# Kernel tuning notes

Hardware: AMD Instinct MI355X
Metric: run time of the kernel (lower is better)

Reference implementation:

```python
import jax, jax.numpy as jnp
import numpy as np

HEAD_SIZE = 128
N_EMBED = 2048
B, T = 4, 4096


def setup_inputs() -> dict:
    key = jax.random.key(0)
    kx, kq, kk, kv = jax.random.split(key, 4)
    s = 1.0 / np.sqrt(N_EMBED)
    return {
        "x": jax.random.normal(kx, (B, T, N_EMBED), dtype=jnp.float32),
        "Wq": jax.random.normal(kq, (N_EMBED, HEAD_SIZE), dtype=jnp.float32) * s,
        "Wk": jax.random.normal(kk, (N_EMBED, HEAD_SIZE), dtype=jnp.float32) * s,
        "Wv": jax.random.normal(kv, (N_EMBED, HEAD_SIZE), dtype=jnp.float32) * s,
    }


def reference(x, Wq, Wk, Wv):
    # x: [B, T, C]; projections (no bias)
    q = jnp.einsum('btc,cd->btd', x, Wq)  # [B, T, D]
    k = jnp.einsum('btc,cd->btd', x, Wk)
    v = jnp.einsum('btc,cd->btd', x, Wv)
    scale = q.shape[-1] ** -0.5
    scores = jnp.einsum('btd,bsd->bts', q, k) * scale  # [B, T, T]
    T_ = x.shape[1]
    causal = jnp.tril(jnp.ones((T_, T_), dtype=bool))
    scores = jnp.where(causal, scores, -jnp.inf)
    weight = jax.nn.softmax(scores, axis=-1)
    # dropout is identity in eval mode
    out = jnp.einsum('bts,bsd->btd', weight, v)  # [B, T, D]
    return out
```

## Files before the change

### kernel.cpp

```cpp
#include <hip/hip_runtime.h>
#include <hip/hip_bf16.h>
#include <stdint.h>

typedef unsigned short ushort_t;
typedef short v8s __attribute__((ext_vector_type(8)));
typedef float f32x4 __attribute__((ext_vector_type(4)));
typedef float f32x16 __attribute__((ext_vector_type(16)));

#define MFMA16(a, b, c) __builtin_amdgcn_mfma_f32_16x16x32_bf16(a, b, c, 0, 0, 0)
#define MFMA32(a, b, c) __builtin_amdgcn_mfma_f32_32x32x16_bf16(a, b, c, 0, 0, 0)

typedef __attribute__((address_space(1))) void gvoid;
typedef __attribute__((address_space(3))) void svoid;

__device__ __forceinline__ void gld16(const void* g, void* s) {
    __builtin_amdgcn_global_load_lds((gvoid*)g, (svoid*)s, 16, 0, 0);
}

__device__ __forceinline__ ushort_t f2bf(float f) {
    union { __hip_bfloat16 b; ushort_t u; } c;
    c.b = __float2bfloat16(f);
    return c.u;
}

__device__ __forceinline__ unsigned f2bf2(float a, float b) {
    union { __hip_bfloat162 b2; unsigned u; } c;
    c.b2 = __float22bfloat162_rn(make_float2(a, b));
    return c.u;
}

__global__ void transpose_w(const float* __restrict__ Wq, const float* __restrict__ Wk,
                            const float* __restrict__ Wv, ushort_t* __restrict__ WT) {
    __shared__ float tile[64][132];
    int bid = blockIdx.x;
    int w = bid >> 5;
    int k0 = (bid & 31) << 6;
    const float* W = (w == 0) ? Wq : ((w == 1) ? Wk : Wv);
    int tid = threadIdx.x;
    #pragma unroll
    for (int i = 0; i < 8; i++) {
        int row = i * 8 + (tid >> 5);
        int col = (tid & 31) * 4;
        float4 v = *(const float4*)(W + (size_t)(k0 + row) * 128 + col);
        tile[row][col] = v.x; tile[row][col + 1] = v.y;
        tile[row][col + 2] = v.z; tile[row][col + 3] = v.w;
    }
    __syncthreads();
    int n = tid >> 1, kh = (tid & 1) * 32;
    ushort_t* dst = WT + ((size_t)(w * 128 + n)) * 2048 + k0 + kh;
    #pragma unroll
    for (int j = 0; j < 32; j += 4) {
        union { ushort_t u[4]; uint2 v2; } pk;
        #pragma unroll
        for (int e = 0; e < 4; e++) pk.u[e] = f2bf(tile[kh + j + e][n]);
        *(uint2*)(dst + j) = pk.v2;
    }
}

#define PJ_XLOAD(S, IT)                                                       \
    {                                                                         \
        _Pragma("unroll")                                                     \
        for (int i = 0; i < 4; i++)                                           \
            S[i] = *(const f32x4*)(xsrc[i] + (size_t)(IT) * 256);             \
    }

#define PJ_CVT_WRITE(RS, PAR)                                                 \
    {                                                                         \
        _Pragma("unroll")                                                     \
        for (int i = 0; i < 4; i++) {                                         \
            uint2 p;                                                          \
            p.x = f2bf2(RS[i][0], RS[i][1]);                                  \
            p.y = f2bf2(RS[i][2], RS[i][3]);                                  \
            *(uint2*)((char*)abuf + (PAR) * 16384 + awb[i]) = p;              \
        }                                                                     \
    }

#define PJ_PHASE1(PAR, IT, DOB)                                               \
    {                                                                         \
        const char* ab = (const char*)abuf + (PAR) * 16384;                   \
        const char* bb = (const char*)bbuf + (PAR) * 24576;                   \
        v8s af[4], bf[3];                                                     \
        _Pragma("unroll")                                                     \
        for (int m = 0; m < 4; m++) {                                         \
            int row = wr * 64 + m * 16 + lr;                                  \
            af[m] = *(const v8s*)(ab + row * 128 + ((lg * 16) ^ ((row & 7) << 4))); \
        }                                                                     \
        _Pragma("unroll")                                                     \
        for (int n = 0; n < 3; n++) {                                         \
            int row = wc * 48 + n * 16 + lr;                                  \
            bf[n] = *(const v8s*)(bb + row * 128 + ((lg * 16) ^ ((row & 7) << 4))); \
        }                                                                     \
        __builtin_amdgcn_sched_barrier(0);                                    \
        if (DOB) {                                                            \
            _Pragma("unroll")                                                 \
            for (int i = 0; i < 3; i++)                                       \
                gld16(bsrc[i] + (size_t)((IT) + 1) * 128,                     \
                      (char*)bbuf + ((PAR) ^ 1) * 24576 + (wid * 3 + i) * 1024); \
        }                                                                     \
        __builtin_amdgcn_sched_barrier(0);                                    \
        __builtin_amdgcn_s_barrier();                                         \
        asm volatile("s_waitcnt lgkmcnt(0)" ::: "memory");                    \
        __builtin_amdgcn_sched_barrier(0);                                    \
        __builtin_amdgcn_s_setprio(1);                                        \
        _Pragma("unroll")                                                     \
        for (int m = 0; m < 4; m++)                                           \
            _Pragma("unroll")                                                 \
            for (int n = 0; n < 3; n++)                                       \
                acc[m][n] = MFMA16(af[m], bf[n], acc[m][n]);                  \
        __builtin_amdgcn_s_setprio(0);                                        \
        __builtin_amdgcn_s_barrier();                                         \
    }

#define PJ_PHASE2(PAR, IT, RLOAD, RCVT, DOX, DOB)                             \
    {                                                                         \
        const char* ab = (const char*)abuf + (PAR) * 16384;                   \
        const char* bb = (const char*)bbuf + (PAR) * 24576;                   \
        v8s af[4], bf[3];                                                     \
        _Pragma("unroll")                                                     \
        for (int m = 0; m < 4; m++) {                                         \
            int row = wr * 64 + m * 16 + lr;                                  \
            af[m] = *(const v8s*)(ab + row * 128 + ((64 + lg * 16) ^ ((row & 7) << 4))); \
        }                                                                     \
        _Pragma("unroll")                                                     \
        for (int n = 0; n < 3; n++) {                                         \
            int row = wc * 48 + n * 16 + lr;                                  \
            bf[n] = *(const v8s*)(bb + row * 128 + ((64 + lg * 16) ^ ((row & 7) << 4))); \
        }                                                                     \
        __builtin_amdgcn_sched_barrier(0);                                    \
        if (DOX) PJ_XLOAD(RLOAD, (IT) + 2);                                   \
        __builtin_amdgcn_sched_barrier(0);                                    \
        if (DOB) PJ_CVT_WRITE(RCVT, (PAR) ^ 1);                               \
        __builtin_amdgcn_sched_barrier(0);                                    \
        if (DOB) {                                                            \
            if (DOX) { asm volatile("s_waitcnt vmcnt(4)" ::: "memory"); }     \
            else     { asm volatile("s_waitcnt vmcnt(0)" ::: "memory"); }     \
        }                                                                     \
        __builtin_amdgcn_s_barrier();                                         \
        asm volatile("s_waitcnt lgkmcnt(0)" ::: "memory");                    \
        __builtin_amdgcn_sched_barrier(0);                                    \
        __builtin_amdgcn_s_setprio(1);                                        \
        _Pragma("unroll")                                                     \
        for (int m = 0; m < 4; m++)                                           \
            _Pragma("unroll")                                                 \
            for (int n = 0; n < 3; n++)                                       \
                acc[m][n] = MFMA16(af[m], bf[n], acc[m][n]);                  \
        __builtin_amdgcn_s_setprio(0);                                        \
        __builtin_amdgcn_s_barrier();                                         \
    }

#define PJ_TILE(PAR, IT, RLOAD, RCVT, DOX, DOB)                               \
    PJ_PHASE1(PAR, IT, DOB)                                                   \
    PJ_PHASE2(PAR, IT, RLOAD, RCVT, DOX, DOB)

__launch_bounds__(512, 1)
__global__ void proj_kernel(const float* __restrict__ x, const ushort_t* __restrict__ WT,
                            ushort_t* __restrict__ q, ushort_t* __restrict__ kb,
                            ushort_t* __restrict__ vb) {
    __shared__ ushort_t abuf[2][8192];
    __shared__ ushort_t bbuf[2][12288];

    int bid = blockIdx.x;
    int xcd = bid & 7, t2 = bid >> 3;
    int nh = t2 & 1, mtl = t2 >> 1;
    int mtile = xcd * 16 + mtl;
    size_t m0 = (size_t)mtile * 128;
    int c0 = nh * 192;
    int tid = threadIdx.x, lane = tid & 63, wid = tid >> 6;
    int lg = lane >> 4, lr = lane & 15;
    int wr = wid >> 2, wc = wid & 3;

    f32x4 acc[4][3];
    #pragma unroll
    for (int m = 0; m < 4; m++)
        #pragma unroll
        for (int n = 0; n < 3; n++) acc[m][n] = (f32x4){0.f, 0.f, 0.f, 0.f};

    const char* xsrc[4];
    int awb[4];
    #pragma unroll
    for (int i = 0; i < 4; i++) {
        int row = 16 * wid + 4 * i + (lane >> 4);
        xsrc[i] = (const char*)x + (m0 + row) * 8192 + (lane & 15) * 16;
        awb[i] = row * 128 + (((lane & 15) * 8) ^ ((row & 7) << 4));
    }

    const char* bsrc[3];
    #pragma unroll
    for (int i = 0; i < 3; i++) {
        int row = 8 * (3 * wid + i) + (lane >> 3);
        int col = ((lane & 7) * 16) ^ ((row & 7) << 4);
        bsrc[i] = (const char*)WT + (size_t)(c0 + row) * 4096 + col;
    }

    f32x4 xs0[4], xs1[4];
    #pragma unroll
    for (int i = 0; i < 3; i++)
        gld16(bsrc[i], (char*)bbuf + (wid * 3 + i) * 1024);
    PJ_XLOAD(xs0, 0);
    PJ_XLOAD(xs1, 1);
    PJ_CVT_WRITE(xs0, 0);
    asm volatile("s_waitcnt vmcnt(0)" ::: "memory");
    asm volatile("s_waitcnt lgkmcnt(0)" ::: "memory");
    __builtin_amdgcn_s_barrier();

    for (int t = 0; t < 30; t += 2) {
        PJ_TILE(0, t,     xs0, xs1, 1, 1);
        PJ_TILE(1, t + 1, xs1, xs0, 1, 1);
    }
    PJ_TILE(0, 30, xs0, xs1, 0, 1);
    PJ_TILE(1, 31, xs1, xs0, 0, 0);

    #pragma unroll
    for (int m = 0; m < 4; m++) {
        #pragma unroll
        for (int e = 0; e < 4; e++) {
            size_t row = m0 + (size_t)(wr * 64 + m * 16 + 4 * lg + e);
            int t = (int)(row & 4095);
            size_t base = (row >> 12) * 524288;
            #pragma unroll
            for (int n = 0; n < 3; n++) {
                int col = c0 + wc * 48 + n * 16 + lr;
                int w = col >> 7, d = col & 127;
                ushort_t val = f2bf(acc[m][n][e]);
                if (w == 0)
                    q[base + (size_t)(t >> 5) * 4096 + (d >> 4) * 512 + ((d >> 3) & 1) * 256 + (t & 31) * 8 + (d & 7)] = val;
                else if (w == 1)
                    kb[base + (size_t)(t >> 5) * 4096 + (d >> 4) * 512 + ((d >> 3) & 1) * 256 + (t & 31) * 8 + (d & 7)] = val;
                else
                    vb[base + (size_t)(t >> 4) * 2048 + (d >> 5) * 512 + ((t >> 3) & 1) * 256 + (d & 31) * 8 + (t & 7)] = val;
            }
        }
    }
}

__device__ __forceinline__ f32x16 zero16() {
    f32x16 z;
    #pragma unroll
    for (int i = 0; i < 16; i++) z[i] = 0.f;
    return z;
}

#define ATT_PVC(SV, BASE, VC, CNEXT)                                          \
    {                                                                         \
        unsigned a0 = f2bf2(SV[(BASE) + 0], SV[(BASE) + 1]);                  \
        unsigned a1 = f2bf2(SV[(BASE) + 2], SV[(BASE) + 3]);                  \
        unsigned b0 = f2bf2(SV[(BASE) + 4], SV[(BASE) + 5]);                  \
        unsigned b1 = f2bf2(SV[(BASE) + 6], SV[(BASE) + 7]);                  \
        unsigned snd0 = hi ? a0 : b0, snd1 = hi ? a1 : b1;                    \
        unsigned rcv0 = (unsigned)__shfl_xor((int)snd0, 32);                  \
        unsigned rcv1 = (unsigned)__shfl_xor((int)snd1, 32);                  \
        union { unsigned u[4]; v8s v; } pf;                                   \
        pf.u[0] = hi ? rcv0 : a0;                                             \
        pf.u[1] = hi ? rcv1 : a1;                                             \
        pf.u[2] = hi ? b0 : rcv0;                                             \
        pf.u[3] = hi ? b1 : rcv1;                                             \
        __builtin_amdgcn_s_setprio(1);                                        \
        _Pragma("unroll")                                                     \
        for (int dt = 0; dt < 4; dt++)                                        \
            accO[dt] = MFMA32(VC[dt], pf.v, accO[dt]);                        \
        __builtin_amdgcn_s_setprio(0);                                        \
        if ((CNEXT) >= 0) {                                                   \
            _Pragma("unroll")                                                 \
            for (int dt = 0; dt < 4; dt++)                                    \
                VC[dt] = *(const v8s*)(vg + (CNEXT) * 2048 + dt * 512);       \
        }                                                                     \
    }

__launch_bounds__(256, 2)
__global__ void attn_kernel(const ushort_t* __restrict__ q, const ushort_t* __restrict__ kb,
                            const ushort_t* __restrict__ vb, float* __restrict__ out) {
    __shared__ float obuf[4][4][16][64];
    __shared__ float stat[2][4][64];

    int bid = blockIdx.x;
    int xcd = bid & 7, rk = bid >> 3;
    int b = xcd >> 1;
    int g = rk * 2 + (xcd & 1);
    int qt = (g & 1) ? (g >> 1) : (127 - (g >> 1));
    int qt0 = qt * 32;
    int tid = threadIdx.x, lane = tid & 63, wid = tid >> 6;
    int hi = lane >> 5, lo = lane & 31;
    size_t bb = (size_t)b * 524288;
    int nt = (qt >> 1) + 1;
    const float cexp = 0.08838834764831845f * 1.4426950408889634f;

    v8s qf[8];
    {
        const ushort_t* qg = q + bb + (size_t)qt * 4096 + (size_t)lane * 8;
        #pragma unroll
        for (int ks = 0; ks < 8; ks++) qf[ks] = *(const v8s*)(qg + ks * 512);
    }

    f32x16 accO[4];
    #pragma unroll
    for (int dt = 0; dt < 4; dt++) accO[dt] = zero16();
    float mrun = -1e30f, lrun = 0.f;

    for (int t = wid; t < nt; t += 4) {
        const ushort_t* kg = kb + bb + (size_t)t * 8192 + (size_t)lane * 8;
        const ushort_t* vg = vb + bb + (size_t)t * 8192 + (size_t)lane * 8;

        f32x16 s0 = zero16(), s1 = zero16();
        __builtin_amdgcn_s_setprio(1);
        #pragma unroll
        for (int ks = 0; ks < 8; ks++) {
            v8s kf = *(const v8s*)(kg + ks * 512);
            s0 = MFMA32(kf, qf[ks], s0);
        }
        #pragma unroll
        for (int ks = 0; ks < 8; ks++) {
            v8s kf = *(const v8s*)(kg + 4096 + ks * 512);
            s1 = MFMA32(kf, qf[ks], s1);
        }
        __builtin_amdgcn_s_setprio(0);

        v8s vA[4], vB[4];
        #pragma unroll
        for (int dt = 0; dt < 4; dt++) vA[dt] = *(const v8s*)(vg + dt * 512);
        #pragma unroll
        for (int dt = 0; dt < 4; dt++) vB[dt] = *(const v8s*)(vg + 2048 + dt * 512);

        if (t == nt - 1) {
            int qrow = qt0 + lo;
            #pragma unroll
            for (int r = 0; r < 16; r++) {
                int kvb = t * 64 + (r & 3) + 8 * (r >> 2) + 4 * hi;
                if (kvb > qrow) s0[r] = -1e30f;
                if (kvb + 32 > qrow) s1[r] = -1e30f;
            }
        }

        float mx = s0[0];
        #pragma unroll
        for (int r = 1; r < 16; r++) mx = fmaxf(mx, s0[r]);
        #pragma unroll
        for (int r = 0; r < 16; r++) mx = fmaxf(mx, s1[r]);
        mx = fmaxf(mx, __shfl_xor(mx, 32));

        if (__any(mx > mrun + 62.7f)) {
            float mnew = fmaxf(mrun, mx);
            float fr = exp2f((mrun - mnew) * cexp);
            lrun *= fr;
            #pragma unroll
            for (int dt = 0; dt < 4; dt++)
                #pragma unroll
                for (int r = 0; r < 16; r++) accO[dt][r] *= fr;
            mrun = mnew;
        }
        float mc = mrun * cexp;
        float rs = 0.f;
        #pragma unroll
        for (int r = 0; r < 16; r++) { s0[r] = exp2f(fmaf(s0[r], cexp, -mc)); rs += s0[r]; }
        #pragma unroll
        for (int r = 0; r < 16; r++) { s1[r] = exp2f(fmaf(s1[r], cexp, -mc)); rs += s1[r]; }
        rs += __shfl_xor(rs, 32);
        lrun += rs;

        ATT_PVC(s0, 0, vA, 2);
        ATT_PVC(s0, 8, vB, 3);
        ATT_PVC(s1, 0, vA, -1);
        ATT_PVC(s1, 8, vB, -1);
    }

    #pragma unroll
    for (int dt = 0; dt < 4; dt++)
        #pragma unroll
        for (int r = 0; r < 16; r++)
            obuf[wid][dt][r][lane] = accO[dt][r];
    stat[0][wid][lane] = mrun;
    stat[1][wid][lane] = lrun;
    __syncthreads();

    float m0 = stat[0][0][lane], m1 = stat[0][1][lane];
    float m2 = stat[0][2][lane], m3 = stat[0][3][lane];
    float m = fmaxf(fmaxf(m0, m1), fmaxf(m2, m3));
    float f0 = exp2f((m0 - m) * cexp), f1 = exp2f((m1 - m) * cexp);
    float f2 = exp2f((m2 - m) * cexp), f3 = exp2f((m3 - m) * cexp);
    float lsum = f0 * stat[1][0][lane] + f1 * stat[1][1][lane]
               + f2 * stat[1][2][lane] + f3 * stat[1][3][lane];
    float linv = 1.0f / lsum;

    float o[16];
    #pragma unroll
    for (int r = 0; r < 16; r++)
        o[r] = (f0 * obuf[0][wid][r][lane] + f1 * obuf[1][wid][r][lane]
              + f2 * obuf[2][wid][r][lane] + f3 * obuf[3][wid][r][lane]) * linv;

    float* orow = out + ((size_t)b * 4096 + qt0 + lo) * 128 + wid * 32 + 4 * hi;
    #pragma unroll
    for (int a = 0; a < 4; a++) {
        float4 vv;
        vv.x = o[4 * a + 0]; vv.y = o[4 * a + 1];
        vv.z = o[4 * a + 2]; vv.w = o[4 * a + 3];
        *(float4*)(orow + 8 * a) = vv;
    }
}

extern "C" void kernel_launch(void* const* d_in, const int* in_sizes, int n_in,
                              void* d_out, int out_size, void* d_ws, size_t ws_size,
                              hipStream_t stream) {
    const float* x  = (const float*)d_in[0];
    const float* Wq = (const float*)d_in[1];
    const float* Wk = (const float*)d_in[2];
    const float* Wv = (const float*)d_in[3];
    float* out = (float*)d_out;
    char* ws = (char*)d_ws;

    ushort_t* q  = (ushort_t*)(ws);
    ushort_t* kb = (ushort_t*)(ws + (4u << 20));
    ushort_t* vb = (ushort_t*)(ws + (8u << 20));
    ushort_t* WT = (ushort_t*)(ws + (12u << 20));

    transpose_w<<<dim3(96), dim3(256), 0, stream>>>(Wq, Wk, Wv, WT);
    proj_kernel<<<dim3(256), dim3(512), 0, stream>>>(x, WT, q, kb, vb);
    attn_kernel<<<dim3(512), dim3(256), 0, stream>>>(q, kb, vb, out);
}
```

Before: 91.83 us.

## Triple-buffer weight tiles in projection GEMM to prefetch two iterations ahead

The projection kernel's weight (B) tiles move from a double buffer to a triple buffer in LDS, and each iteration now issues their async global-to-LDS loads two k-steps ahead instead of one. The vmcnt wait is relaxed to allow more outstanding loads, and the bf16 convert-write of x is reordered to follow the wait. The aim is to hide global load latency for the weights behind more MFMA work. The cost is an extra 24 KB of LDS and a more intricate slot rotation that has to stay consistent with the wait counts.

```diff
diff --git a/kernel.cpp b/kernel.cpp
--- a/kernel.cpp
+++ b/kernel.cpp
@@ -75,10 +75,10 @@
         }                                                                     \
     }
 
-#define PJ_PHASE1(PAR, IT, DOB)                                               \
+#define PJ_PHASE1(APAR, BSLOT, BNSLOT, IT, DOB2)                              \
     {                                                                         \
-        const char* ab = (const char*)abuf + (PAR) * 16384;                   \
-        const char* bb = (const char*)bbuf + (PAR) * 24576;                   \
+        const char* ab = (const char*)abuf + (APAR) * 16384;                  \
+        const char* bb = (const char*)bbuf + (BSLOT) * 24576;                 \
         v8s af[4], bf[3];                                                     \
         _Pragma("unroll")                                                     \
         for (int m = 0; m < 4; m++) {                                         \
@@ -91,11 +91,11 @@
             bf[n] = *(const v8s*)(bb + row * 128 + ((lg * 16) ^ ((row & 7) << 4))); \
         }                                                                     \
         __builtin_amdgcn_sched_barrier(0);                                    \
-        if (DOB) {                                                            \
+        if (DOB2) {                                                           \
             _Pragma("unroll")                                                 \
             for (int i = 0; i < 3; i++)                                       \
-                gld16(bsrc[i] + (size_t)((IT) + 1) * 128,                     \
-                      (char*)bbuf + ((PAR) ^ 1) * 24576 + (wid * 3 + i) * 1024); \
+                gld16(bsrc[i] + (size_t)((IT) + 2) * 128,                     \
+                      (char*)bbuf + (BNSLOT) * 24576 + (wid * 3 + i) * 1024); \
         }                                                                     \
         __builtin_amdgcn_sched_barrier(0);                                    \
         __builtin_amdgcn_s_barrier();                                         \
@@ -111,10 +111,10 @@
         __builtin_amdgcn_s_barrier();                                         \
     }
 
-#define PJ_PHASE2(PAR, IT, RLOAD, RCVT, DOX, DOB)                             \
+#define PJ_PHASE2(APAR, BSLOT, IT, RLOAD, RCVT, DOX2, DOCVT, VMN)             \
     {                                                                         \
-        const char* ab = (const char*)abuf + (PAR) * 16384;                   \
-        const char* bb = (const char*)bbuf + (PAR) * 24576;                   \
+        const char* ab = (const char*)abuf + (APAR) * 16384;                  \
+        const char* bb = (const char*)bbuf + (BSLOT) * 24576;                 \
         v8s af[4], bf[3];                                                     \
         _Pragma("unroll")                                                     \
         for (int m = 0; m < 4; m++) {                                         \
@@ -127,14 +127,13 @@
             bf[n] = *(const v8s*)(bb + row * 128 + ((64 + lg * 16) ^ ((row & 7) << 4))); \
         }                                                                     \
         __builtin_amdgcn_sched_barrier(0);                                    \
-        if (DOX) PJ_XLOAD(RLOAD, (IT) + 2);                                   \
-        __builtin_amdgcn_sched_barrier(0);                                    \
-        if (DOB) PJ_CVT_WRITE(RCVT, (PAR) ^ 1);                               \
-        __builtin_amdgcn_sched_barrier(0);                                    \
-        if (DOB) {                                                            \
-            if (DOX) { asm volatile("s_waitcnt vmcnt(4)" ::: "memory"); }     \
-            else     { asm volatile("s_waitcnt vmcnt(0)" ::: "memory"); }     \
-        }                                                                     \
+        if (DOX2) PJ_XLOAD(RLOAD, (IT) + 2);                                  \
+        __builtin_amdgcn_sched_barrier(0);                                    \
+        if ((VMN) == 7) { asm volatile("s_waitcnt vmcnt(7)" ::: "memory"); }  \
+        else if ((VMN) == 0) { asm volatile("s_waitcnt vmcnt(0)" ::: "memory"); } \
+        __builtin_amdgcn_sched_barrier(0);                                    \
+        if (DOCVT) PJ_CVT_WRITE(RCVT, (APAR) ^ 1);                            \
+        __builtin_amdgcn_sched_barrier(0);                                    \
         __builtin_amdgcn_s_barrier();                                         \
         asm volatile("s_waitcnt lgkmcnt(0)" ::: "memory");                    \
         __builtin_amdgcn_sched_barrier(0);                                    \
@@ -148,16 +147,16 @@
         __builtin_amdgcn_s_barrier();                                         \
     }
 
-#define PJ_TILE(PAR, IT, RLOAD, RCVT, DOX, DOB)                               \
-    PJ_PHASE1(PAR, IT, DOB)                                                   \
-    PJ_PHASE2(PAR, IT, RLOAD, RCVT, DOX, DOB)
+#define PJ_TILE(APAR, BSLOT, BNSLOT, IT, RLOAD, RCVT, DOB2, DOX2, DOCVT, VMN) \
+    PJ_PHASE1(APAR, BSLOT, BNSLOT, IT, DOB2)                                  \
+    PJ_PHASE2(APAR, BSLOT, IT, RLOAD, RCVT, DOX2, DOCVT, VMN)
 
 __launch_bounds__(512, 1)
 __global__ void proj_kernel(const float* __restrict__ x, const ushort_t* __restrict__ WT,
                             ushort_t* __restrict__ q, ushort_t* __restrict__ kb,
                             ushort_t* __restrict__ vb) {
     __shared__ ushort_t abuf[2][8192];
-    __shared__ ushort_t bbuf[2][12288];
+    __shared__ ushort_t bbuf[3][12288];
 
     int bid = blockIdx.x;
     int xcd = bid & 7, t2 = bid >> 3;
@@ -196,19 +195,26 @@
     #pragma unroll
     for (int i = 0; i < 3; i++)
         gld16(bsrc[i], (char*)bbuf + (wid * 3 + i) * 1024);
+    #pragma unroll
+    for (int i = 0; i < 3; i++)
+        gld16(bsrc[i] + 128, (char*)bbuf + 24576 + (wid * 3 + i) * 1024);
     PJ_XLOAD(xs0, 0);
     PJ_XLOAD(xs1, 1);
+    asm volatile("s_waitcnt vmcnt(4)" ::: "memory");
     PJ_CVT_WRITE(xs0, 0);
-    asm volatile("s_waitcnt vmcnt(0)" ::: "memory");
     asm volatile("s_waitcnt lgkmcnt(0)" ::: "memory");
     __builtin_amdgcn_s_barrier();
 
-    for (int t = 0; t < 30; t += 2) {
-        PJ_TILE(0, t,     xs0, xs1, 1, 1);
-        PJ_TILE(1, t + 1, xs1, xs0, 1, 1);
-    }
-    PJ_TILE(0, 30, xs0, xs1, 0, 1);
-    PJ_TILE(1, 31, xs1, xs0, 0, 0);
+    for (int t6 = 0; t6 < 30; t6 += 6) {
+        PJ_TILE(0, 0, 2, t6 + 0, xs0, xs1, 1, 1, 1, 7);
+        PJ_TILE(1, 1, 0, t6 + 1, xs1, xs0, 1, 1, 1, 7);
+        PJ_TILE(0, 2, 1, t6 + 2, xs0, xs1, 1, 1, 1, 7);
+        PJ_TILE(1, 0, 2, t6 + 3, xs1, xs0, 1, 1, 1, 7);
+        PJ_TILE(0, 1, 0, t6 + 4, xs0, xs1, 1, 1, 1, 7);
+        PJ_TILE(1, 2, 1, t6 + 5, xs1, xs0, 1, 1, 1, 7);
+    }
+    PJ_TILE(0, 0, 0, 30, xs0, xs1, 0, 0, 1, 0);
+    PJ_TILE(1, 1, 0, 31, xs1, xs0, 0, 0, 0, -1);
 
     #pragma unroll
     for (int m = 0; m < 4; m++) {
```

After: 91.70 us. No clear change (-0.1%).

## Pre-convert x to blocked bf16 and project with register-direct MFMA kernel

Applied to the files above, without the earlier changes.

Adds an xconvert pass that writes x as bf16 in an MFMA-fragment-blocked layout, and has transpose_w also emit weights in a matching blocked layout. A new projection kernel then loads operand fragments straight from global memory into registers with double buffering and no LDS staging, using 32x32 MFMAs. The aim is to remove LDS traffic and barriers from the projection GEMM. In exchange it adds an extra pass over x (fp32 read plus bf16 write) and a dependency on a large workspace. The old path is kept as a fallback when the workspace is too small.

```diff
diff --git a/kernel.cpp b/kernel.cpp
--- a/kernel.cpp
+++ b/kernel.cpp
@@ -29,8 +29,16 @@
     return c.u;
 }
 
+__device__ __forceinline__ f32x16 zero16() {
+    f32x16 z;
+    #pragma unroll
+    for (int i = 0; i < 16; i++) z[i] = 0.f;
+    return z;
+}
+
 __global__ void transpose_w(const float* __restrict__ Wq, const float* __restrict__ Wk,
-                            const float* __restrict__ Wv, ushort_t* __restrict__ WT) {
+                            const float* __restrict__ Wv, ushort_t* __restrict__ WT,
+                            ushort_t* __restrict__ WB) {
     __shared__ float tile[64][132];
     int bid = blockIdx.x;
     int w = bid >> 5;
@@ -47,13 +55,132 @@
     }
     __syncthreads();
     int n = tid >> 1, kh = (tid & 1) * 32;
-    ushort_t* dst = WT + ((size_t)(w * 128 + n)) * 2048 + k0 + kh;
+    int dg = w * 128 + n;
+    ushort_t* dst = WT + (size_t)dg * 2048 + k0 + kh;
     #pragma unroll
     for (int j = 0; j < 32; j += 4) {
         union { ushort_t u[4]; uint2 v2; } pk;
         #pragma unroll
         for (int e = 0; e < 4; e++) pk.u[e] = f2bf(tile[kh + j + e][n]);
         *(uint2*)(dst + j) = pk.v2;
+    }
+    ushort_t* db = WB + (size_t)(dg >> 5) * 65536 + (dg & 31) * 8;
+    #pragma unroll
+    for (int o = 0; o < 4; o++) {
+        int K = k0 + kh + o * 8;
+        union { ushort_t u[8]; v8s v; } pk8;
+        #pragma unroll
+        for (int e = 0; e < 8; e++) pk8.u[e] = f2bf(tile[kh + o * 8 + e][n]);
+        *(v8s*)(db + (size_t)(K >> 4) * 512 + ((K >> 3) & 1) * 256) = pk8.v;
+    }
+}
+
+__launch_bounds__(256, 2)
+__global__ void xconvert(const float* __restrict__ x, ushort_t* __restrict__ xb) {
+    __shared__ ushort_t lbuf[16384];
+    int tt = blockIdx.x;
+    int tid = threadIdx.x;
+    const float* xs = x + (size_t)tt * 32 * 2048;
+    ushort_t* xd = xb + (size_t)tt * 65536;
+    for (int c = 0; c < 4; c++) {
+        if (c) __syncthreads();
+        #pragma unroll
+        for (int j = 0; j < 16; j++) {
+            int f = tid + j * 256;
+            int row = f >> 7;
+            int kl = (f & 127) * 4;
+            float4 v = *(const float4*)(xs + (size_t)row * 2048 + c * 512 + kl);
+            uint2 p;
+            p.x = f2bf2(v.x, v.y);
+            p.y = f2bf2(v.z, v.w);
+            *(uint2*)(lbuf + (kl >> 4) * 512 + ((kl >> 3) & 1) * 256 + row * 8 + (kl & 7)) = p;
+        }
+        __syncthreads();
+        #pragma unroll
+        for (int j = 0; j < 8; j++) {
+            int off = tid * 8 + j * 2048;
+            *(v8s*)(xd + c * 16384 + off) = *(const v8s*)(lbuf + off);
+        }
+    }
+}
+
+#define PB_LOAD(WF, XA, XB2, C)                                               \
+    {                                                                         \
+        _Pragma("unroll")                                                     \
+        for (int j = 0; j < 4; j++) WF[j]  = *(const v8s*)(wg  + ((C) * 4 + j) * 512); \
+        _Pragma("unroll")                                                     \
+        for (int j = 0; j < 4; j++) XA[j]  = *(const v8s*)(xg0 + ((C) * 4 + j) * 512); \
+        _Pragma("unroll")                                                     \
+        for (int j = 0; j < 4; j++) XB2[j] = *(const v8s*)(xg1 + ((C) * 4 + j) * 512); \
+    }
+
+#define PB_STEP(WF, XA, XB2)                                                  \
+    {                                                                         \
+        __builtin_amdgcn_s_setprio(1);                                        \
+        _Pragma("unroll")                                                     \
+        for (int j = 0; j < 4; j++) {                                         \
+            acc0 = MFMA32(WF[j], XA[j], acc0);                                \
+            acc1 = MFMA32(WF[j], XB2[j], acc1);                               \
+        }                                                                     \
+        __builtin_amdgcn_s_setprio(0);                                        \
+    }
+
+__launch_bounds__(384, 3)
+__global__ void proj_blk(const ushort_t* __restrict__ xb, const ushort_t* __restrict__ wb,
+                         ushort_t* __restrict__ q, ushort_t* __restrict__ kb,
+                         ushort_t* __restrict__ vb) {
+    int bid = blockIdx.x;
+    int xcd = bid & 7, idx = bid >> 3;
+    int dblk = idx & 3, tbl = idx >> 2;
+    int tb = (xcd * 16 + tbl) * 128;
+    int tid = threadIdx.x, lane = tid & 63, wid = tid >> 6;
+    int dw = wid % 3, th = wid / 3;
+    int d0 = dblk * 96 + dw * 32;
+    int hi = lane >> 5, lo = lane & 31;
+
+    const ushort_t* xg0 = xb + (size_t)((tb >> 5) + th * 2) * 65536 + lane * 8;
+    const ushort_t* xg1 = xg0 + 65536;
+    const ushort_t* wg  = wb + (size_t)(d0 >> 5) * 65536 + lane * 8;
+
+    f32x16 acc0 = zero16(), acc1 = zero16();
+    v8s wfA[4], xaA[4], xbA[4], wfB[4], xaB[4], xbB[4];
+
+    PB_LOAD(wfA, xaA, xbA, 0);
+    for (int c = 0; c < 30; c += 2) {
+        PB_LOAD(wfB, xaB, xbB, c + 1);
+        PB_STEP(wfA, xaA, xbA);
+        PB_LOAD(wfA, xaA, xbA, c + 2);
+        PB_STEP(wfB, xaB, xbB);
+    }
+    PB_LOAD(wfB, xaB, xbB, 31);
+    PB_STEP(wfA, xaA, xbA);
+    PB_STEP(wfB, xaB, xbB);
+
+    int w = d0 >> 7;
+    int ddb = d0 & 127;
+    size_t bbase = (size_t)(tb >> 12) * 524288;
+    int tloc = (tb & 4095) + th * 64;
+    #pragma unroll
+    for (int tt2 = 0; tt2 < 2; tt2++) {
+        f32x16 A = tt2 ? acc1 : acc0;
+        int ttile = (tloc >> 5) + tt2;
+        if (w < 2) {
+            ushort_t* dst = (w == 0) ? q : kb;
+            size_t tbase = bbase + (size_t)ttile * 4096 + lo * 8;
+            #pragma unroll
+            for (int r = 0; r < 16; r++) {
+                int d = ddb + (r & 3) + 8 * (r >> 2) + 4 * hi;
+                dst[tbase + (d >> 4) * 512 + ((d >> 3) & 1) * 256 + (d & 7)] = f2bf(A[r]);
+            }
+        } else {
+            int t = ttile * 32 + lo;
+            size_t tbase = bbase + (size_t)(t >> 4) * 2048 + ((t >> 3) & 1) * 256 + (t & 7);
+            #pragma unroll
+            for (int r = 0; r < 16; r++) {
+                int d = ddb + (r & 3) + 8 * (r >> 2) + 4 * hi;
+                vb[tbase + (d >> 5) * 512 + (d & 31) * 8] = f2bf(A[r]);
+            }
+        }
     }
 }
 
@@ -153,9 +280,9 @@
     PJ_PHASE2(PAR, IT, RLOAD, RCVT, DOX, DOB)
 
 __launch_bounds__(512, 1)
-__global__ void proj_kernel(const float* __restrict__ x, const ushort_t* __restrict__ WT,
-                            ushort_t* __restrict__ q, ushort_t* __restrict__ kb,
-                            ushort_t* __restrict__ vb) {
+__global__ void proj_fb(const float* __restrict__ x, const ushort_t* __restrict__ WT,
+                        ushort_t* __restrict__ q, ushort_t* __restrict__ kb,
+                        ushort_t* __restrict__ vb) {
     __shared__ ushort_t abuf[2][8192];
     __shared__ ushort_t bbuf[2][12288];
 
@@ -183,7 +310,6 @@
         xsrc[i] = (const char*)x + (m0 + row) * 8192 + (lane & 15) * 16;
         awb[i] = row * 128 + (((lane & 15) * 8) ^ ((row & 7) << 4));
     }
-
     const char* bsrc[3];
     #pragma unroll
     for (int i = 0; i < 3; i++) {
@@ -233,13 +359,6 @@
     }
 }
 
-__device__ __forceinline__ f32x16 zero16() {
-    f32x16 z;
-    #pragma unroll
-    for (int i = 0; i < 16; i++) z[i] = 0.f;
-    return z;
-}
-
 #define ATT_PVC(SV, BASE, VC, CNEXT)                                          \
     {                                                                         \
         unsigned a0 = f2bf2(SV[(BASE) + 0], SV[(BASE) + 1]);                  \
@@ -410,8 +529,15 @@
     ushort_t* kb = (ushort_t*)(ws + (4u << 20));
     ushort_t* vb = (ushort_t*)(ws + (8u << 20));
     ushort_t* WT = (ushort_t*)(ws + (12u << 20));
-
-    transpose_w<<<dim3(96), dim3(256), 0, stream>>>(Wq, Wk, Wv, WT);
-    proj_kernel<<<dim3(256), dim3(512), 0, stream>>>(x, WT, q, kb, vb);
+    ushort_t* WB = (ushort_t*)(ws + (14u << 20));
+    ushort_t* xb = (ushort_t*)(ws + (16u << 20));
+
+    transpose_w<<<dim3(96), dim3(256), 0, stream>>>(Wq, Wk, Wv, WT, WB);
+    if (ws_size >= (80ull << 20)) {
+        xconvert<<<dim3(512), dim3(256), 0, stream>>>(x, xb);
+        proj_blk<<<dim3(512), dim3(384), 0, stream>>>(xb, WB, q, kb, vb);
+    } else {
+        proj_fb<<<dim3(256), dim3(512), 0, stream>>>(x, WT, q, kb, vb);
+    }
     attn_kernel<<<dim3(512), dim3(256), 0, stream>>>(q, kb, vb, out);
 }
```

Measured after the change: 145.2 us. 58.1% more time.
